# Kernel tuning notes

Hardware: AMD Instinct MI355X
Metric: run time of the kernel (lower is better)

The kernel has to match this reference:

```python
import jax, jax.numpy as jnp
import numpy as np

EPS = 1e-5
D_STATE = 16
D_INNER = 2
D_CONV = 4


def batchnorm(x, g, b):
    # BatchNorm1d in training mode: biased batch statistics over the batch dim
    m = x.mean(axis=0)
    v = x.var(axis=0)
    return g * (x - m) * jax.lax.rsqrt(v + EPS) + b


def mamba(u, W_in, conv_w, conv_b, W_xproj, W_dt, b_dt, A_log, D, W_out):
    # u: [B, L, 1] (d_model=1, d_inner=2, d_state=16, dt_rank=1)
    Bsz, L, _ = u.shape
    xz = jnp.einsum('bld,ed->ble', u, W_in)            # [B,L,4]
    x, z = jnp.split(xz, 2, axis=-1)                    # [B,L,2] each
    # causal depthwise conv along L
    xc = jnp.transpose(x, (0, 2, 1))                    # [B,C,L]
    xc = jax.lax.conv_general_dilated(
        xc, conv_w, (1,), [(D_CONV - 1, 0)],
        dimension_numbers=('NCH', 'OIH', 'NCH'),
        feature_group_count=D_INNER)
    x = jax.nn.silu(jnp.transpose(xc, (0, 2, 1)) + conv_b)  # [B,L,2]
    x_dbl = jnp.einsum('ble,fe->blf', x, W_xproj)       # [B,L,1+2*16]
    dt = jax.nn.softplus(jnp.einsum('blr,er->ble', x_dbl[..., :1], W_dt) + b_dt)  # [B,L,2]
    Bm = x_dbl[..., 1:1 + D_STATE]                      # [B,L,16]
    Cm = x_dbl[..., 1 + D_STATE:1 + 2 * D_STATE]        # [B,L,16]
    A = -jnp.exp(A_log)                                 # [2,16]

    def step(h, inp):
        dt_t, B_t, C_t, x_t = inp                       # [B,2],[B,16],[B,16],[B,2]
        dA = jnp.exp(dt_t[:, :, None] * A)              # [B,2,16]
        h = h * dA + dt_t[:, :, None] * B_t[:, None, :] * x_t[:, :, None]
        y = jnp.einsum('ben,bn->be', h, C_t) + D * x_t
        return h, y

    h0 = jnp.zeros((Bsz, D_INNER, D_STATE), u.dtype)
    xs = (dt.transpose(1, 0, 2), Bm.transpose(1, 0, 2),
          Cm.transpose(1, 0, 2), x.transpose(1, 0, 2))
    _, ys = jax.lax.scan(step, h0, xs)                  # [L,B,2]
    y = ys.transpose(1, 0, 2) * jax.nn.silu(z)          # [B,L,2]
    return jnp.einsum('ble,de->bld', y, W_out)          # [B,L,1]


def setup_inputs() -> dict:
    key = jax.random.key(0)
    ks = jax.random.split(key, 16)
    B = 1024
    s = 0.02
    inp = {
        'x': jax.random.normal(ks[0], (B, 1775), jnp.float32),
        'W1': jax.random.normal(ks[1], (2048, 1775), jnp.float32) * s,
        'g1': jnp.ones((2048,), jnp.float32),
        'b1': jnp.zeros((2048,), jnp.float32),
        'W_in': jax.random.normal(ks[2], (2 * D_INNER, 1), jnp.float32) * s,
        'conv_w': jax.random.normal(ks[3], (D_INNER, 1, D_CONV), jnp.float32) * 0.2,
        'conv_b': jnp.zeros((D_INNER,), jnp.float32),
        'W_xproj': jax.random.normal(ks[4], (1 + 2 * D_STATE, D_INNER), jnp.float32) * 0.2,
        'W_dt': jax.random.normal(ks[5], (D_INNER, 1), jnp.float32) * 0.2,
        'b_dt': jax.random.normal(ks[6], (D_INNER,), jnp.float32) * 0.2,
        'A_log': jnp.tile(jnp.log(jnp.arange(1, D_STATE + 1, dtype=jnp.float32)), (D_INNER, 1)),
        'D': jnp.ones((D_INNER,), jnp.float32),
        'W_out': jax.random.normal(ks[7], (1, D_INNER), jnp.float32) * 0.2,
        'W2': jax.random.normal(ks[8], (512, 2048), jnp.float32) * s,
        'g2': jnp.ones((512,), jnp.float32),
        'b2': jnp.zeros((512,), jnp.float32),
        'W3': jax.random.normal(ks[9], (256, 512), jnp.float32) * s,
    }
    return inp


def reference(x, W1, g1, b1, W_in, conv_w, conv_b, W_xproj, W_dt, b_dt,
              A_log, D, W_out, W2, g2, b2, W3):
    h = batchnorm(x @ W1.T, g1, b1)                     # [B,2048]
    h = mamba(h[:, :, None], W_in, conv_w, conv_b, W_xproj, W_dt, b_dt,
              A_log, D, W_out)[:, :, 0]                 # [B,2048]
    h = jax.nn.relu(batchnorm(h @ W2.T, g2, b2))        # [B,512]
    return h @ W3.T                                     # [B,256]
```

## Files before the change

kernel.cpp:

```cpp
#include <hip/hip_runtime.h>
#include <math.h>

#define SEQL 2048
#define BATCH 1024
#define CHUNK 64
#define NCH 32

typedef _Float16 f16x8 __attribute__((ext_vector_type(8)));
typedef _Float16 f16x4 __attribute__((ext_vector_type(4)));
typedef _Float16 h2 __attribute__((ext_vector_type(2)));
typedef float f32x4 __attribute__((ext_vector_type(4)));

__device__ inline unsigned short f2h(float f) {
    _Float16 h = (_Float16)f;
    return *reinterpret_cast<unsigned short*>(&h);
}
__device__ inline float packh2(float a, float b) {
    return __uint_as_float((unsigned)f2h(a) | ((unsigned)f2h(b) << 16));
}
__device__ inline float hext(float packed, int sh) {
    const unsigned short s = (unsigned short)(__float_as_uint(packed) >> sh);
    _Float16 h = *reinterpret_cast<const _Float16*>(&s);
    return (float)h;
}

__device__ inline void gl2lds16(const void* g, void* l) {
    __builtin_amdgcn_global_load_lds(
        (const __attribute__((address_space(1))) unsigned int*)g,
        (__attribute__((address_space(3))) unsigned int*)l, 16, 0, 0);
}

template<int CTRL>
__device__ inline float dppadd(float v) {
    const int p = __builtin_amdgcn_update_dpp(0, __float_as_int(v), CTRL, 0xF, 0xF, true);
    return v + __int_as_float(p);
}

__global__ __launch_bounds__(256) void cvt_all(
    const float* __restrict__ x, const float* __restrict__ W1,
    const float* __restrict__ W2, const float* __restrict__ W3,
    _Float16* __restrict__ xh, _Float16* __restrict__ w1h,
    _Float16* __restrict__ w2h, _Float16* __restrict__ w3h)
{
    const int bid = blockIdx.x;
    if (bid < 3072) {
        const float* src; _Float16* dst;
        if (bid < 1024) { src = x + (size_t)bid * 1775;           dst = xh  + (size_t)bid * 1792; }
        else            { src = W1 + (size_t)(bid - 1024) * 1775; dst = w1h + (size_t)(bid - 1024) * 1792; }
        f16x4* dst4 = reinterpret_cast<f16x4*>(dst);
        for (int i = threadIdx.x; i < 448; i += 256) {
            const int k = i * 4;
            float4 v = {0.f, 0.f, 0.f, 0.f};
            if (k + 3 < 1775) v = *reinterpret_cast<const float4*>(&src[k]);
            else {
                if (k     < 1775) v.x = src[k];
                if (k + 1 < 1775) v.y = src[k + 1];
                if (k + 2 < 1775) v.z = src[k + 2];
            }
            f16x4 o; o[0] = (_Float16)v.x; o[1] = (_Float16)v.y; o[2] = (_Float16)v.z; o[3] = (_Float16)v.w;
            dst4[i] = o;
        }
    } else {
        const float* src; _Float16* dst; int nvec;
        if (bid < 3584) { const int r = bid - 3072; src = W2 + (size_t)r * 2048; dst = w2h + (size_t)r * 2048; nvec = 512; }
        else            { const int r = bid - 3584; src = W3 + (size_t)r * 512;  dst = w3h + (size_t)r * 512;  nvec = 128; }
        f16x4* dst4 = reinterpret_cast<f16x4*>(dst);
        for (int i = threadIdx.x; i < nvec; i += 256) {
            const float4 v = reinterpret_cast<const float4*>(src)[i];
            f16x4 o; o[0] = (_Float16)v.x; o[1] = (_Float16)v.y; o[2] = (_Float16)v.z; o[3] = (_Float16)v.w;
            dst4[i] = o;
        }
    }
}

__global__ __launch_bounds__(256) void cvt_bnrelu(
    const float* __restrict__ P0, const float* __restrict__ P1,
    const float* __restrict__ sc, const float* __restrict__ tc,
    _Float16* __restrict__ h3)
{
    const int row = blockIdx.x * 2 + (threadIdx.x >> 7);
    const int i = threadIdx.x & 127;
    const float4 p0 = reinterpret_cast<const float4*>(P0 + (size_t)row * 512)[i];
    const float4 p1 = reinterpret_cast<const float4*>(P1 + (size_t)row * 512)[i];
    const float4 sv = reinterpret_cast<const float4*>(sc)[i];
    const float4 tv = reinterpret_cast<const float4*>(tc)[i];
    f16x4 o;
    o[0] = (_Float16)fmaxf(fmaf(sv.x, p0.x + p1.x, tv.x), 0.f);
    o[1] = (_Float16)fmaxf(fmaf(sv.y, p0.y + p1.y, tv.y), 0.f);
    o[2] = (_Float16)fmaxf(fmaf(sv.z, p0.z + p1.z, tv.z), 0.f);
    o[3] = (_Float16)fmaxf(fmaf(sv.w, p0.w + p1.w, tv.w), 0.f);
    reinterpret_cast<f16x4*>(h3 + (size_t)row * 512)[i] = o;
}

__global__ __launch_bounds__(256) void gemm_f16(
    const _Float16* __restrict__ A, const _Float16* __restrict__ B,
    float* __restrict__ C, int ldc, int Kp, int ksteps, size_t coff,
    float* __restrict__ bnp, int bn_ld)
{
    __shared__ __attribute__((aligned(16))) _Float16 sA[64 * 64];
    __shared__ __attribute__((aligned(16))) _Float16 sB[64 * 64];

    const int tid = threadIdx.x;
    const int wave = tid >> 6;
    const int lane = tid & 63;
    const int m0 = blockIdx.y * 64;
    const int n0 = blockIdx.x * 64;
    C += (size_t)blockIdx.z * coff;

    const int srow = tid >> 3;
    const int pslot = tid & 7;
    const int gslot = pslot ^ (srow & 7);
    const size_t gk0 = (size_t)blockIdx.z * ksteps * 64 + gslot * 8;
    const _Float16* gA0 = A + (size_t)(m0 + srow) * Kp + gk0;
    const _Float16* gA1 = A + (size_t)(m0 + 32 + srow) * Kp + gk0;
    const _Float16* gB0 = B + (size_t)(n0 + srow) * Kp + gk0;
    const _Float16* gB1 = B + (size_t)(n0 + 32 + srow) * Kp + gk0;
    const int wdst = wave * 512;

    const int wr = wave >> 1, wc = wave & 1;
    const int li = lane & 15, gq = lane >> 4;
    const int p0s = (gq    ) ^ (li & 7);
    const int p1s = (gq + 4) ^ (li & 7);

    f32x4 acc[2][2];
    #pragma unroll
    for (int i = 0; i < 2; ++i)
        #pragma unroll
        for (int j = 0; j < 2; ++j)
            #pragma unroll
            for (int v = 0; v < 4; ++v) acc[i][j][v] = 0.f;

    for (int kt = 0; kt < ksteps; ++kt) {
        const size_t go = (size_t)kt * 64;
        gl2lds16(gA0 + go, &sA[wdst]);
        gl2lds16(gA1 + go, &sA[2048 + wdst]);
        gl2lds16(gB0 + go, &sB[wdst]);
        gl2lds16(gB1 + go, &sB[2048 + wdst]);
        __syncthreads();

        f16x8 af[2][2], bg[2][2];
        #pragma unroll
        for (int mi = 0; mi < 2; ++mi) {
            const int rb = (wr * 32 + mi * 16 + li) * 64;
            af[mi][0] = *(const f16x8*)&sA[rb + p0s * 8];
            af[mi][1] = *(const f16x8*)&sA[rb + p1s * 8];
        }
        #pragma unroll
        for (int ni = 0; ni < 2; ++ni) {
            const int rb = (wc * 32 + ni * 16 + li) * 64;
            bg[ni][0] = *(const f16x8*)&sB[rb + p0s * 8];
            bg[ni][1] = *(const f16x8*)&sB[rb + p1s * 8];
        }
        #pragma unroll
        for (int mi = 0; mi < 2; ++mi)
            #pragma unroll
            for (int ni = 0; ni < 2; ++ni) {
                acc[mi][ni] = __builtin_amdgcn_mfma_f32_16x16x32_f16(af[mi][0], bg[ni][0], acc[mi][ni], 0, 0, 0);
                acc[mi][ni] = __builtin_amdgcn_mfma_f32_16x16x32_f16(af[mi][1], bg[ni][1], acc[mi][ni], 0, 0, 0);
            }
        __syncthreads();
    }

    #pragma unroll
    for (int mi = 0; mi < 2; ++mi)
        #pragma unroll
        for (int ni = 0; ni < 2; ++ni) {
            const int col = n0 + wc * 32 + ni * 16 + li;
            #pragma unroll
            for (int i = 0; i < 4; ++i) {
                const int row = m0 + wr * 32 + mi * 16 + gq * 4 + i;
                C[(size_t)row * ldc + col] = acc[mi][ni][i];
            }
        }

    if (bnp) {
        #pragma unroll
        for (int ni = 0; ni < 2; ++ni) {
            float ps = 0.f, pq = 0.f;
            #pragma unroll
            for (int mi = 0; mi < 2; ++mi)
                #pragma unroll
                for (int i = 0; i < 4; ++i) {
                    const float v = acc[mi][ni][i];
                    ps += v; pq += v * v;
                }
            ps += __shfl_xor(ps, 16); ps += __shfl_xor(ps, 32);
            pq += __shfl_xor(pq, 16); pq += __shfl_xor(pq, 32);
            if (gq == 0) {
                const int col = n0 + wc * 32 + ni * 16 + li;
                const int grp = blockIdx.y * 2 + wr;
                bnp[(size_t)(grp * 2    ) * bn_ld + col] = ps;
                bnp[(size_t)(grp * 2 + 1) * bn_ld + col] = pq;
            }
        }
    }
}

__global__ __launch_bounds__(256) void bn_part(
    const float* __restrict__ X, const float* __restrict__ X2,
    int rows_per, int ld, float* __restrict__ part)
{
    __shared__ float rs[4][64], rq[4][64];
    const int tid = threadIdx.x;
    const int c = tid & 63, rg4 = tid >> 6;
    const int col = blockIdx.x * 64 + c;
    const int r0 = blockIdx.y * rows_per;
    float sum = 0.f, sq = 0.f;
    for (int r = rg4; r < rows_per; r += 4) {
        const size_t idx = (size_t)(r0 + r) * ld + col;
        float v = X[idx];
        if (X2) v += X2[idx];
        sum += v; sq += v * v;
    }
    rs[rg4][c] = sum; rq[rg4][c] = sq;
    __syncthreads();
    if (rg4 == 0) {
        sum = rs[0][c] + rs[1][c] + rs[2][c] + rs[3][c];
        sq  = rq[0][c] + rq[1][c] + rq[2][c] + rq[3][c];
        part[((size_t)blockIdx.y * 2    ) * ld + col] = sum;
        part[((size_t)blockIdx.y * 2 + 1) * ld + col] = sq;
    }
}

__global__ __launch_bounds__(256) void bn_fin(
    const float* __restrict__ part, int RG, int ld, float inv_rows,
    const float* __restrict__ g, const float* __restrict__ b,
    float* __restrict__ s, float* __restrict__ t)
{
    const int col = blockIdx.x * 256 + threadIdx.x;
    if (col >= ld) return;
    float sum = 0.f, sq = 0.f;
    for (int z = 0; z < RG; ++z) {
        sum += part[((size_t)z * 2    ) * ld + col];
        sq  += part[((size_t)z * 2 + 1) * ld + col];
    }
    const float mean = sum * inv_rows;
    const float var = fmaxf(sq * inv_rows - mean * mean, 0.f);
    const float rstd = 1.0f / sqrtf(var + 1e-5f);
    const float sv = g[col] * rstd;
    s[col] = sv;
    t[col] = b[col] - mean * sv;
}

__global__ __launch_bounds__(512, 8) void mamba_scan9(
    const float* __restrict__ Y, _Float16* __restrict__ a2,
    const float* __restrict__ s1, const float* __restrict__ t1,
    const float* __restrict__ Win, const float* __restrict__ convw,
    const float* __restrict__ convb, const float* __restrict__ Wx,
    const float* __restrict__ Wdt, const float* __restrict__ bdt,
    const float* __restrict__ Alog, const float* __restrict__ Dp,
    const float* __restrict__ Wout)
{
    __shared__ __align__(16) float4 pk[SEQL];
    __shared__ float Pa[2][NCH][16];
    __shared__ float Sa[2][NCH][16];

    const int tid = threadIdx.x;
    const int row = blockIdx.x;
    const float* yrow = Y + (size_t)row * SEQL;
    _Float16* a2row = a2 + (size_t)row * SEQL;

    {
        const int l0 = tid * 4;
        float4 ym = {0.f,0.f,0.f,0.f}, sm = {0.f,0.f,0.f,0.f}, tm = {0.f,0.f,0.f,0.f};
        if (tid > 0) {
            ym = *reinterpret_cast<const float4*>(&yrow[l0 - 4]);
            sm = *reinterpret_cast<const float4*>(&s1[l0 - 4]);
            tm = *reinterpret_cast<const float4*>(&t1[l0 - 4]);
        }
        const float4 y0 = *reinterpret_cast<const float4*>(&yrow[l0]);
        const float4 s0 = *reinterpret_cast<const float4*>(&s1[l0]);
        const float4 t0 = *reinterpret_cast<const float4*>(&t1[l0]);

        float ua[8];
        ua[0] = fmaf(sm.x, ym.x, tm.x);
        ua[1] = fmaf(sm.y, ym.y, tm.y);
        ua[2] = fmaf(sm.z, ym.z, tm.z);
        ua[3] = fmaf(sm.w, ym.w, tm.w);
        ua[4] = fmaf(s0.x, y0.x, t0.x);
        ua[5] = fmaf(s0.y, y0.y, t0.y);
        ua[6] = fmaf(s0.z, y0.z, t0.z);
        ua[7] = fmaf(s0.w, y0.w, t0.w);

        const float wi0 = Win[0], wi1 = Win[1];
        const float wz0 = Win[2], wz1 = Win[3];
        const float wo0 = Wout[0], wo1 = Wout[1];
        const float cw00 = convw[0], cw01 = convw[1], cw02 = convw[2], cw03 = convw[3];
        const float cw10 = convw[4], cw11 = convw[5], cw12 = convw[6], cw13 = convw[7];
        const float cb0 = convb[0], cb1 = convb[1];
        const float wx00 = Wx[0], wx01 = Wx[1];
        const float wdt0 = Wdt[0], wdt1 = Wdt[1];
        const float bdt0 = bdt[0], bdt1 = bdt[1];

        #pragma unroll
        for (int j = 0; j < 4; ++j) {
            const int l = l0 + j;
            const float u0 = ua[j + 4], um1 = ua[j + 3], um2 = ua[j + 2], um3 = ua[j + 1];
            const float c0 = fmaf(wi0, cw00 * um3 + cw01 * um2 + cw02 * um1 + cw03 * u0, cb0);
            const float c1 = fmaf(wi1, cw10 * um3 + cw11 * um2 + cw12 * um1 + cw13 * u0, cb1);
            const float xs0 = c0 / (1.f + __expf(-c0));
            const float xs1 = c1 / (1.f + __expf(-c1));
            const float d0 = xs0 * wx00 + xs1 * wx01;
            const float dt0 = __logf(1.f + __expf(fmaf(d0, wdt0, bdt0)));
            const float dt1 = __logf(1.f + __expf(fmaf(d0, wdt1, bdt1)));
            const float z0 = u0 * wz0, z1 = u0 * wz1;
            const float g0 = (z0 / (1.f + __expf(-z0))) * wo0;
            const float g1 = (z1 / (1.f + __expf(-z1))) * wo1;
            float4 rec;
            rec.x = dt0; rec.y = dt1;
            rec.z = packh2(xs0, xs1);
            rec.w = packh2(g0, g1);
            pk[((l & 63) << 5) + (l >> 6)] = rec;
        }
    }
    __syncthreads();

    const int ch = tid >> 4;
    const int n  = tid & 15;

    const float A0 = -__expf(Alog[n])      * 1.44269504f;
    const float A1 = -__expf(Alog[16 + n]) * 1.44269504f;
    h2 wxB2, wxC2;
    wxB2[0] = (_Float16)Wx[(1 + n) * 2 + 0];
    wxB2[1] = (_Float16)Wx[(1 + n) * 2 + 1];
    wxC2[0] = (_Float16)Wx[(17 + n) * 2 + 0];
    wxC2[1] = (_Float16)Wx[(17 + n) * 2 + 1];

    {
        float h0 = 0.f, h1 = 0.f, p0 = 1.f, p1 = 1.f;
        for (int i0 = 0; i0 < CHUNK; i0 += 8) {
            #pragma unroll
            for (int j = 0; j < 8; ++j) {
                const float4 v = pk[((i0 + j) << 5) + ch];
                const h2 xs2 = __builtin_bit_cast(h2, v.z);
                const float Bn = __builtin_amdgcn_fdot2(xs2, wxB2, 0.f, false);
                const float xs0 = hext(v.z, 0), xs1 = hext(v.z, 16);
                const float dA0 = __builtin_amdgcn_exp2f(v.x * A0);
                const float dA1 = __builtin_amdgcn_exp2f(v.y * A1);
                h0 = fmaf(h0, dA0, (v.x * xs0) * Bn);
                h1 = fmaf(h1, dA1, (v.y * xs1) * Bn);
                p0 *= dA0; p1 *= dA1;
            }
        }
        Pa[0][ch][n] = p0; Pa[1][ch][n] = p1;
        Sa[0][ch][n] = h0; Sa[1][ch][n] = h1;
    }
    __syncthreads();

    if (tid < 32) {
        const int e = tid >> 4, nn = tid & 15;
        float H = 0.f;
        #pragma unroll
        for (int cc = 0; cc < NCH; ++cc) {
            const float Pv = Pa[e][cc][nn];
            const float Sv = Sa[e][cc][nn];
            Sa[e][cc][nn] = H;
            H = fmaf(Pv, H, Sv);
        }
    }
    __syncthreads();

    {
        h2 D2h;
        D2h[0] = (_Float16)Dp[0];
        D2h[1] = (_Float16)Dp[1];
        const int base = ch * CHUNK;
        float h0 = Sa[0][ch][n], h1 = Sa[1][ch][n];
        for (int i0 = 0; i0 < CHUNK; i0 += 8) {
            float qs[8];
            #pragma unroll
            for (int j = 0; j < 8; ++j) {
                const float4 v = pk[((i0 + j) << 5) + ch];
                const h2 xs2 = __builtin_bit_cast(h2, v.z);
                const h2 gg2 = __builtin_bit_cast(h2, v.w);
                const float Bn = __builtin_amdgcn_fdot2(xs2, wxB2, 0.f, false);
                const float Cn = __builtin_amdgcn_fdot2(xs2, wxC2, 0.f, false);
                const float xs0 = hext(v.z, 0), xs1 = hext(v.z, 16);
                const float g0 = hext(v.w, 0),  g1 = hext(v.w, 16);
                const float dA0 = __builtin_amdgcn_exp2f(v.x * A0);
                const float dA1 = __builtin_amdgcn_exp2f(v.y * A1);
                h0 = fmaf(h0, dA0, (v.x * xs0) * Bn);
                h1 = fmaf(h1, dA1, (v.y * xs1) * Bn);
                float t = h0 * g0;
                t = fmaf(h1, g1, t);
                float q = t * Cn;
                q = dppadd<0xB1>(q);
                q = dppadd<0x4E>(q);
                q = dppadd<0x141>(q);
                q = dppadd<0x140>(q);
                const h2 dgh = D2h * gg2;
                const float dterm = __builtin_amdgcn_fdot2(xs2, dgh, 0.f, false);
                qs[j] = q + dterm;
            }
            if (n == 0) {
                float4 st;
                st.x = __builtin_bit_cast(float, __builtin_amdgcn_cvt_pkrtz(qs[0], qs[1]));
                st.y = __builtin_bit_cast(float, __builtin_amdgcn_cvt_pkrtz(qs[2], qs[3]));
                st.z = __builtin_bit_cast(float, __builtin_amdgcn_cvt_pkrtz(qs[4], qs[5]));
                st.w = __builtin_bit_cast(float, __builtin_amdgcn_cvt_pkrtz(qs[6], qs[7]));
                *reinterpret_cast<float4*>(&a2row[base + i0]) = st;
            }
        }
    }
}

extern "C" void kernel_launch(void* const* d_in, const int* in_sizes, int n_in,
                              void* d_out, int out_size, void* d_ws, size_t ws_size,
                              hipStream_t stream)
{
    const float* x     = (const float*)d_in[0];
    const float* W1    = (const float*)d_in[1];
    const float* g1    = (const float*)d_in[2];
    const float* b1    = (const float*)d_in[3];
    const float* Win   = (const float*)d_in[4];
    const float* convw = (const float*)d_in[5];
    const float* convb = (const float*)d_in[6];
    const float* Wx    = (const float*)d_in[7];
    const float* Wdt   = (const float*)d_in[8];
    const float* bdt   = (const float*)d_in[9];
    const float* Alog  = (const float*)d_in[10];
    const float* Dp    = (const float*)d_in[11];
    const float* Wout  = (const float*)d_in[12];
    const float* W2    = (const float*)d_in[13];
    const float* g2    = (const float*)d_in[14];
    const float* b2    = (const float*)d_in[15];
    const float* W3    = (const float*)d_in[16];

    unsigned char* base = (unsigned char*)d_ws;
    float* C1 = (float*)(base + 0);
    float* P0 = (float*)(base + 8388608);
    float* P1 = (float*)(base + 10485760);
    float* s1 = (float*)(base + 12582912);
    float* t1 = (float*)(base + 12591104);
    float* s2 = (float*)(base + 12599296);
    float* t2 = (float*)(base + 12601344);
    float* bnp = (float*)(base + 12615680);
    _Float16* a2  = (_Float16*)(base + 13172736);
    _Float16* xh  = (_Float16*)(base + 17367040);
    _Float16* w1h = (_Float16*)(base + 21037056);
    _Float16* w2h = (_Float16*)(base + 28377088);
    _Float16* w3h = (_Float16*)(base + 30474240);
    _Float16* h3h = (_Float16*)(base + 30736384);

    cvt_all<<<3840, 256, 0, stream>>>(x, W1, W2, W3, xh, w1h, w2h, w3h);

    gemm_f16<<<dim3(32, 16, 1), 256, 0, stream>>>(
        xh, w1h, C1, 2048, 1792, 28, 0, bnp, 2048);

    bn_fin<<<8, 256, 0, stream>>>(bnp, 32, 2048, 1.0f / 1024.f, g1, b1, s1, t1);

    mamba_scan9<<<1024, 512, 0, stream>>>(C1, a2, s1, t1, Win, convw, convb,
                                          Wx, Wdt, bdt, Alog, Dp, Wout);

    gemm_f16<<<dim3(8, 16, 2), 256, 0, stream>>>(
        a2, w2h, P0, 512, 2048, 16, (size_t)1024 * 512, nullptr, 0);

    bn_part<<<dim3(8, 16), 256, 0, stream>>>(P0, P1, 64, 512, bnp);
    bn_fin<<<2, 256, 0, stream>>>(bnp, 16, 512, 1.0f / 1024.f, g2, b2, s2, t2);

    cvt_bnrelu<<<512, 256, 0, stream>>>(P0, P1, s2, t2, h3h);

    gemm_f16<<<dim3(4, 16, 1), 256, 0, stream>>>(
        h3h, w3h, (float*)d_out, 256, 512, 8, 0, nullptr, 0);
}
```

Before: 127.6 us.

## Double-buffer GEMM LDS tiles and drop split-K for second GEMM with fused BN stats

```diff
diff --git a/kernel.cpp b/kernel.cpp
--- a/kernel.cpp
+++ b/kernel.cpp
@@ -74,43 +74,41 @@
 }
 
 __global__ __launch_bounds__(256) void cvt_bnrelu(
-    const float* __restrict__ P0, const float* __restrict__ P1,
+    const float* __restrict__ P0,
     const float* __restrict__ sc, const float* __restrict__ tc,
     _Float16* __restrict__ h3)
 {
     const int row = blockIdx.x * 2 + (threadIdx.x >> 7);
     const int i = threadIdx.x & 127;
     const float4 p0 = reinterpret_cast<const float4*>(P0 + (size_t)row * 512)[i];
-    const float4 p1 = reinterpret_cast<const float4*>(P1 + (size_t)row * 512)[i];
     const float4 sv = reinterpret_cast<const float4*>(sc)[i];
     const float4 tv = reinterpret_cast<const float4*>(tc)[i];
     f16x4 o;
-    o[0] = (_Float16)fmaxf(fmaf(sv.x, p0.x + p1.x, tv.x), 0.f);
-    o[1] = (_Float16)fmaxf(fmaf(sv.y, p0.y + p1.y, tv.y), 0.f);
-    o[2] = (_Float16)fmaxf(fmaf(sv.z, p0.z + p1.z, tv.z), 0.f);
-    o[3] = (_Float16)fmaxf(fmaf(sv.w, p0.w + p1.w, tv.w), 0.f);
+    o[0] = (_Float16)fmaxf(fmaf(sv.x, p0.x, tv.x), 0.f);
+    o[1] = (_Float16)fmaxf(fmaf(sv.y, p0.y, tv.y), 0.f);
+    o[2] = (_Float16)fmaxf(fmaf(sv.z, p0.z, tv.z), 0.f);
+    o[3] = (_Float16)fmaxf(fmaf(sv.w, p0.w, tv.w), 0.f);
     reinterpret_cast<f16x4*>(h3 + (size_t)row * 512)[i] = o;
 }
 
 __global__ __launch_bounds__(256) void gemm_f16(
     const _Float16* __restrict__ A, const _Float16* __restrict__ B,
-    float* __restrict__ C, int ldc, int Kp, int ksteps, size_t coff,
+    float* __restrict__ C, int ldc, int Kp, int ksteps,
     float* __restrict__ bnp, int bn_ld)
 {
-    __shared__ __attribute__((aligned(16))) _Float16 sA[64 * 64];
-    __shared__ __attribute__((aligned(16))) _Float16 sB[64 * 64];
+    __shared__ __attribute__((aligned(16))) _Float16 sA[2][64 * 64];
+    __shared__ __attribute__((aligned(16))) _Float16 sB[2][64 * 64];
 
     const int tid = threadIdx.x;
     const int wave = tid >> 6;
     const int lane = tid & 63;
     const int m0 = blockIdx.y * 64;
     const int n0 = blockIdx.x * 64;
-    C += (size_t)blockIdx.z * coff;
 
     const int srow = tid >> 3;
     const int pslot = tid & 7;
     const int gslot = pslot ^ (srow & 7);
-    const size_t gk0 = (size_t)blockIdx.z * ksteps * 64 + gslot * 8;
+    const size_t gk0 = (size_t)gslot * 8;
     const _Float16* gA0 = A + (size_t)(m0 + srow) * Kp + gk0;
     const _Float16* gA1 = A + (size_t)(m0 + 32 + srow) * Kp + gk0;
     const _Float16* gB0 = B + (size_t)(n0 + srow) * Kp + gk0;
@@ -130,26 +128,37 @@
             #pragma unroll
             for (int v = 0; v < 4; ++v) acc[i][j][v] = 0.f;
 
+    {
+        gl2lds16(gA0, &sA[0][wdst]);
+        gl2lds16(gA1, &sA[0][2048 + wdst]);
+        gl2lds16(gB0, &sB[0][wdst]);
+        gl2lds16(gB1, &sB[0][2048 + wdst]);
+    }
+    __syncthreads();
+
+    int cur = 0;
     for (int kt = 0; kt < ksteps; ++kt) {
-        const size_t go = (size_t)kt * 64;
-        gl2lds16(gA0 + go, &sA[wdst]);
-        gl2lds16(gA1 + go, &sA[2048 + wdst]);
-        gl2lds16(gB0 + go, &sB[wdst]);
-        gl2lds16(gB1 + go, &sB[2048 + wdst]);
-        __syncthreads();
+        if (kt + 1 < ksteps) {
+            const size_t go = (size_t)(kt + 1) * 64;
+            const int nb = cur ^ 1;
+            gl2lds16(gA0 + go, &sA[nb][wdst]);
+            gl2lds16(gA1 + go, &sA[nb][2048 + wdst]);
+            gl2lds16(gB0 + go, &sB[nb][wdst]);
+            gl2lds16(gB1 + go, &sB[nb][2048 + wdst]);
+        }
 
         f16x8 af[2][2], bg[2][2];
         #pragma unroll
         for (int mi = 0; mi < 2; ++mi) {
             const int rb = (wr * 32 + mi * 16 + li) * 64;
-            af[mi][0] = *(const f16x8*)&sA[rb + p0s * 8];
-            af[mi][1] = *(const f16x8*)&sA[rb + p1s * 8];
+            af[mi][0] = *(const f16x8*)&sA[cur][rb + p0s * 8];
+            af[mi][1] = *(const f16x8*)&sA[cur][rb + p1s * 8];
         }
         #pragma unroll
         for (int ni = 0; ni < 2; ++ni) {
             const int rb = (wc * 32 + ni * 16 + li) * 64;
-            bg[ni][0] = *(const f16x8*)&sB[rb + p0s * 8];
-            bg[ni][1] = *(const f16x8*)&sB[rb + p1s * 8];
+            bg[ni][0] = *(const f16x8*)&sB[cur][rb + p0s * 8];
+            bg[ni][1] = *(const f16x8*)&sB[cur][rb + p1s * 8];
         }
         #pragma unroll
         for (int mi = 0; mi < 2; ++mi)
@@ -159,6 +168,7 @@
                 acc[mi][ni] = __builtin_amdgcn_mfma_f32_16x16x32_f16(af[mi][1], bg[ni][1], acc[mi][ni], 0, 0, 0);
             }
         __syncthreads();
+        cur ^= 1;
     }
 
     #pragma unroll
@@ -193,32 +203,6 @@
                 bnp[(size_t)(grp * 2 + 1) * bn_ld + col] = pq;
             }
         }
-    }
-}
-
-__global__ __launch_bounds__(256) void bn_part(
-    const float* __restrict__ X, const float* __restrict__ X2,
-    int rows_per, int ld, float* __restrict__ part)
-{
-    __shared__ float rs[4][64], rq[4][64];
-    const int tid = threadIdx.x;
-    const int c = tid & 63, rg4 = tid >> 6;
-    const int col = blockIdx.x * 64 + c;
-    const int r0 = blockIdx.y * rows_per;
-    float sum = 0.f, sq = 0.f;
-    for (int r = rg4; r < rows_per; r += 4) {
-        const size_t idx = (size_t)(r0 + r) * ld + col;
-        float v = X[idx];
-        if (X2) v += X2[idx];
-        sum += v; sq += v * v;
-    }
-    rs[rg4][c] = sum; rq[rg4][c] = sq;
-    __syncthreads();
-    if (rg4 == 0) {
-        sum = rs[0][c] + rs[1][c] + rs[2][c] + rs[3][c];
-        sq  = rq[0][c] + rq[1][c] + rq[2][c] + rq[3][c];
-        part[((size_t)blockIdx.y * 2    ) * ld + col] = sum;
-        part[((size_t)blockIdx.y * 2 + 1) * ld + col] = sq;
     }
 }
 
@@ -429,7 +413,6 @@
     unsigned char* base = (unsigned char*)d_ws;
     float* C1 = (float*)(base + 0);
     float* P0 = (float*)(base + 8388608);
-    float* P1 = (float*)(base + 10485760);
     float* s1 = (float*)(base + 12582912);
     float* t1 = (float*)(base + 12591104);
     float* s2 = (float*)(base + 12599296);
@@ -444,22 +427,21 @@
 
     cvt_all<<<3840, 256, 0, stream>>>(x, W1, W2, W3, xh, w1h, w2h, w3h);
 
-    gemm_f16<<<dim3(32, 16, 1), 256, 0, stream>>>(
-        xh, w1h, C1, 2048, 1792, 28, 0, bnp, 2048);
+    gemm_f16<<<dim3(32, 16), 256, 0, stream>>>(
+        xh, w1h, C1, 2048, 1792, 28, bnp, 2048);
 
     bn_fin<<<8, 256, 0, stream>>>(bnp, 32, 2048, 1.0f / 1024.f, g1, b1, s1, t1);
 
     mamba_scan9<<<1024, 512, 0, stream>>>(C1, a2, s1, t1, Win, convw, convb,
                                           Wx, Wdt, bdt, Alog, Dp, Wout);
 
-    gemm_f16<<<dim3(8, 16, 2), 256, 0, stream>>>(
-        a2, w2h, P0, 512, 2048, 16, (size_t)1024 * 512, nullptr, 0);
-
-    bn_part<<<dim3(8, 16), 256, 0, stream>>>(P0, P1, 64, 512, bnp);
-    bn_fin<<<2, 256, 0, stream>>>(bnp, 16, 512, 1.0f / 1024.f, g2, b2, s2, t2);
-
-    cvt_bnrelu<<<512, 256, 0, stream>>>(P0, P1, s2, t2, h3h);
-
-    gemm_f16<<<dim3(4, 16, 1), 256, 0, stream>>>(
-        h3h, w3h, (float*)d_out, 256, 512, 8, 0, nullptr, 0);
-}
+    gemm_f16<<<dim3(8, 16), 256, 0, stream>>>(
+        a2, w2h, P0, 512, 2048, 32, bnp, 512);
+
+    bn_fin<<<2, 256, 0, stream>>>(bnp, 32, 512, 1.0f / 1024.f, g2, b2, s2, t2);
+
+    cvt_bnrelu<<<512, 256, 0, stream>>>(P0, s2, t2, h3h);
+
+    gemm_f16<<<dim3(4, 16), 256, 0, stream>>>(
+        h3h, w3h, (float*)d_out, 256, 512, 8, nullptr, 0);
+}
```

Result: slower. 132.2 us (+3.7%).
